# Performance work log

Measured on AMD Instinct MI355X. Metric: run time of the kernel, lower is better.

Reference implementation:

```python
import jax, jax.numpy as jnp
import numpy as np

B, S, E, H = 4, 2048, 2048, 16
D = E // H  # head_dim = 128
MAX_LEN = 2048


def _make_freqs():
    # standard RoPE frequencies: theta = 10000^{-2i/D}
    inv_freq = 1.0 / (10000.0 ** (np.arange(0, D, 2, dtype=np.float32) / D))  # [D/2]
    t = np.arange(MAX_LEN, dtype=np.float32)
    ang = np.outer(t, inv_freq)  # [max_len, D/2]
    cos = ang.reshape(1, MAX_LEN, 1, D // 2)
    return jnp.asarray(np.cos(cos)), jnp.asarray(np.sin(cos))


def setup_inputs() -> dict:
    key = jax.random.key(0)
    ks = jax.random.split(key, 10)
    sc = 1.0 / np.sqrt(E)
    freqs_cos, freqs_sin = _make_freqs()
    return {
        "x": jax.random.normal(ks[0], (B, S, E), dtype=jnp.float32),
        "freqs_cos": freqs_cos,
        "freqs_sin": freqs_sin,
        "wq": jax.random.normal(ks[1], (E, E), dtype=jnp.float32) * sc,
        "bq": jax.random.normal(ks[2], (E,), dtype=jnp.float32) * 0.01,
        "wk": jax.random.normal(ks[3], (E, E), dtype=jnp.float32) * sc,
        "bk": jax.random.normal(ks[4], (E,), dtype=jnp.float32) * 0.01,
        "wv": jax.random.normal(ks[5], (E, E), dtype=jnp.float32) * sc,
        "bv": jax.random.normal(ks[6], (E,), dtype=jnp.float32) * 0.01,
        "wo": jax.random.normal(ks[7], (E, E), dtype=jnp.float32) * sc,
        "bo": jax.random.normal(ks[8], (E,), dtype=jnp.float32) * 0.01,
    }


def _rope(t, cos, sin):
    # t: [B, S, H, D]; complex multiply on interleaved (even, odd) pairs
    tr = t.reshape(*t.shape[:-1], -1, 2)  # [B,S,H,D/2,2]
    xr, xi = tr[..., 0], tr[..., 1]
    rr = xr * cos - xi * sin
    ri = xr * sin + xi * cos
    return jnp.stack([rr, ri], axis=-1).reshape(t.shape)


def reference(x, freqs_cos, freqs_sin, wq, bq, wk, bk, wv, bv, wo, bo):
    b, s, _ = x.shape
    q = (x @ wq.T + bq).reshape(b, s, H, D)
    k = (x @ wk.T + bk).reshape(b, s, H, D)
    v = (x @ wv.T + bv).reshape(b, s, H, D)
    cos, sin = freqs_cos[:, :s], freqs_sin[:, :s]
    q = _rope(q, cos, sin)
    k = _rope(k, cos, sin)
    # FAITHFUL to source: q,k,v stay [B,S,H,D], so matmul contracts over D
    # producing per-position head-head scores [B,S,H,H] (no transpose to BHSD).
    qk = jnp.einsum("bshd,bsgd->bshg", q, k) / jnp.sqrt(jnp.float32(D))
    att = jax.nn.softmax(qk, axis=-1)
    att_out = jnp.einsum("bshg,bsgd->bshd", att, v)  # [B,S,H,D]
    # torch: transpose(1,2).contiguous().view(B,S,-1) -> h-major flatten
    att_out = jnp.transpose(att_out, (0, 2, 1, 3)).reshape(b, s, -1)
    return att_out @ wo.T + bo
```

## Files before the change

### kernel.cpp

```cpp
#include <hip/hip_runtime.h>
#include <stdint.h>

typedef unsigned short u16t;
typedef __attribute__((ext_vector_type(8))) short frag8;
typedef __attribute__((ext_vector_type(4))) float facc4;

#define S_LEN 2048
#define E_DIM 2048

__device__ __forceinline__ u16t f2bf(float f) {
    union { float f; uint32_t u; } c; c.f = f;
    return (u16t)((c.u + 0x7fffu + ((c.u >> 16) & 1u)) >> 16);
}

__global__ __launch_bounds__(256) void cvt_kernel(const float* __restrict__ src,
                                                  u16t* __restrict__ dst, int n4) {
    int i = blockIdx.x * 256 + threadIdx.x;
    if (i >= n4) return;
    float4 v = ((const float4*)src)[i];
    ushort4 o;
    o.x = f2bf(v.x); o.y = f2bf(v.y); o.z = f2bf(v.z); o.w = f2bf(v.w);
    ((ushort4*)dst)[i] = o;
}

__device__ __forceinline__ void gldl16(const u16t* g, u16t* l) {
    __builtin_amdgcn_global_load_lds(
        (__attribute__((address_space(1))) void*)(g),
        (__attribute__((address_space(3))) void*)(l), 16, 0, 0);
}

__device__ __forceinline__ void gemm256(const u16t* __restrict__ A,
                                        const u16t* __restrict__ B,
                                        int bm0, int bn0,
                                        u16t* L, facc4 acc[8][4]) {
    const int t     = threadIdx.x;
    const int lane  = t & 63;
    const int wid   = t >> 6;
    const int m16   = lane & 15;
    const int quad  = lane >> 4;
    const int wid_m = wid >> 2;
    const int wid_n = wid & 3;

#pragma unroll
    for (int i = 0; i < 8; ++i)
#pragma unroll
        for (int j = 0; j < 4; ++j) acc[i][j] = facc4{0.f, 0.f, 0.f, 0.f};

    const int colA = (((wid_m << 2) + quad) ^ (m16 & 7)) << 3;
    const int colB = ((((wid_n >> 1) << 2) + quad) ^ (m16 & 7)) << 3;
    const int roA  = m16 * 64 + colA;
    const int roB  = ((wid_n & 1) * 64 + m16) * 64 + colB;

    const int cp    = (lane & 7) ^ (lane >> 3);
    const int rgrp  = cp >> 2;
    const int qq    = cp & 3;
    const int line0 = wid * 8 + (lane >> 3);
    const u16t* pA[2]; const u16t* pB[2];
    const int dOf0 = wid * 512;
    const int dOf1 = 4096 + wid * 512;
#pragma unroll
    for (int ld = 0; ld < 2; ++ld) {
        const int grow = rgrp * 128 + ld * 64 + line0;
        pA[ld] = A + (size_t)(bm0 + grow) * E_DIM + qq * 8;
        pB[ld] = B + (size_t)(bn0 + grow) * E_DIM + qq * 8;
    }

#define STG(P, K, DST) { gldl16(P[0] + (K), (DST) + dOf0); \
                         gldl16(P[1] + (K), (DST) + dOf1); }
#define CBAR { asm volatile("" ::: "memory"); \
               __builtin_amdgcn_s_barrier(); \
               asm volatile("" ::: "memory"); }
#define RDB(BASE) { _Pragma("unroll") \
    for (int j = 0; j < 4; ++j) bv[j] = *(const frag8*)((BASE) + roB + j * 1024); }
#define RDA0(BASE) { _Pragma("unroll") \
    for (int i = 0; i < 4; ++i) av[i] = *(const frag8*)((BASE) + roA + i * 1024); }
#define RDA4(BASE) { _Pragma("unroll") \
    for (int i = 0; i < 4; ++i) av[i] = *(const frag8*)((BASE) + roA + (i + 4) * 1024); }
#define MFMA16(IB) { __builtin_amdgcn_s_setprio(1); \
    _Pragma("unroll") for (int i = 0; i < 4; ++i) \
    _Pragma("unroll") for (int j = 0; j < 4; ++j) \
        acc[i + IB][j] = __builtin_amdgcn_mfma_f32_16x16x32_bf16( \
            av[i], bv[j], acc[i + IB][j], 0, 0, 0); \
    __builtin_amdgcn_s_setprio(0); }

    STG(pB, 0,  L + 16384)
    STG(pA, 0,  L + 0)
    STG(pB, 32, L + 24576)
    STG(pA, 32, L + 8192)
    STG(pB, 64, L + 32768 + 16384)
    STG(pA, 64, L + 32768)
    STG(pB, 96, L + 32768 + 24576)
    asm volatile("s_waitcnt vmcnt(6)" ::: "memory");
    CBAR

#pragma unroll 1
    for (int u = 0; u < 16; ++u) {
        const int kO1 = u * 128 + 96;
        const int kE2 = (u < 15) ? u * 128 + 128 : 0;
        const int kO2 = (u < 15) ? u * 128 + 192 : 0;
        frag8 av[4], bv[4];

        RDB(L + 16384) RDA0(L)
        STG(pA, kO1, L + 32768 + 8192)
        CBAR MFMA16(0) CBAR

        RDA4(L)
        STG(pB, kE2, L + 16384)
        CBAR MFMA16(4) CBAR

        RDB(L + 24576) RDA0(L + 8192)
        STG(pA, kE2, L)
        CBAR MFMA16(0) CBAR

        RDA4(L + 8192)
        STG(pB, kE2 + 32, L + 24576)
        asm volatile("s_waitcnt vmcnt(6)" ::: "memory");
        CBAR MFMA16(4) CBAR

        RDB(L + 32768 + 16384) RDA0(L + 32768)
        STG(pA, kE2 + 32, L + 8192)
        CBAR MFMA16(0) CBAR

        RDA4(L + 32768)
        STG(pB, kO2, L + 32768 + 16384)
        CBAR MFMA16(4) CBAR

        RDB(L + 32768 + 24576) RDA0(L + 32768 + 8192)
        STG(pA, kO2, L + 32768)
        CBAR MFMA16(0) CBAR

        RDA4(L + 32768 + 8192)
        STG(pB, kO2 + 32, L + 32768 + 24576)
        asm volatile("s_waitcnt vmcnt(6)" ::: "memory");
        CBAR MFMA16(4) CBAR
    }

    asm volatile("s_waitcnt vmcnt(0)" ::: "memory");

#undef STG
#undef CBAR
#undef RDB
#undef RDA0
#undef RDA4
#undef MFMA16
}

__device__ __forceinline__ void tile_swz(int& bm0, int& bn0) {
    const int orig = blockIdx.y * 8 + blockIdx.x;
    const int swz  = (orig & 7) * 32 + (orig >> 3);
    bm0 = (swz >> 3) * 256;
    bn0 = (swz & 7) * 256;
}

struct QkvArgs {
    const u16t* w[3];
    const float* bias[3];
    u16t* out[3];
};

__global__ __launch_bounds__(512, 2)
void qkv_gemm(const u16t* __restrict__ xb, QkvArgs args,
              const float* __restrict__ fcos, const float* __restrict__ fsin) {
    __shared__ u16t lds[65536];
    facc4 acc[8][4];
    int bm0, bn0; tile_swz(bm0, bn0);
    const int z = blockIdx.z;
    gemm256(xb, args.w[z], bm0, bn0, lds, acc);

    const int t     = threadIdx.x;
    const int lane  = t & 63;
    const int m16   = lane & 15;
    const int quad  = lane >> 4;
    const int wid   = t >> 6;
    const int wid_m = wid >> 2;
    const int wid_n = wid & 3;
    const bool rope = (z < 2);
    u16t* out = args.out[z];
    const float* bias = args.bias[z];

#pragma unroll
    for (int i = 0; i < 8; ++i) {
#pragma unroll
        for (int j = 0; j < 4; ++j) {
            const int n = bn0 + wid_n * 64 + j * 16 + m16;
            const float bn_ = bias[n];
#pragma unroll
            for (int r = 0; r < 4; ++r) {
                const int m = bm0 + wid_m * 128 + i * 16 + quad * 4 + r;
                float v = acc[i][j][r] + bn_;
                const float part = __shfl_xor(v, 1, 64);
                if (rope) {
                    const int s = m & (S_LEN - 1);
                    const int p = (n & 127) >> 1;
                    const float cs = fcos[s * 64 + p];
                    const float sn = fsin[s * 64 + p];
                    v = (n & 1) ? (part * sn + v * cs) : (v * cs - part * sn);
                }
                out[(size_t)m * E_DIM + n] = f2bf(v);
            }
        }
    }
}

__global__ __launch_bounds__(512, 2)
void out_gemm(const u16t* __restrict__ sh, const u16t* __restrict__ wob,
              const float* __restrict__ bo, float* __restrict__ out) {
    __shared__ u16t lds[65536];
    facc4 acc[8][4];
    int bm0, bn0; tile_swz(bm0, bn0);
    gemm256(sh, wob, bm0, bn0, lds, acc);

    const int t     = threadIdx.x;
    const int lane  = t & 63;
    const int m16   = lane & 15;
    const int quad  = lane >> 4;
    const int wid   = t >> 6;
    const int wid_m = wid >> 2;
    const int wid_n = wid & 3;

#pragma unroll
    for (int i = 0; i < 8; ++i) {
#pragma unroll
        for (int j = 0; j < 4; ++j) {
            const int n = bn0 + wid_n * 64 + j * 16 + m16;
            const float bn_ = bo[n];
#pragma unroll
            for (int r = 0; r < 4; ++r) {
                const int m = bm0 + wid_m * 128 + i * 16 + quad * 4 + r;
                out[(size_t)m * E_DIM + n] = acc[i][j][r] + bn_;
            }
        }
    }
}

__global__ __launch_bounds__(256)
void attn_kernel(const u16t* __restrict__ qb, const u16t* __restrict__ kb,
                 const u16t* __restrict__ vb, u16t* __restrict__ sh) {
    __shared__ u16t Vs[4][16 * 136];
    __shared__ u16t Pt[4][16 * 32];

    const int t    = threadIdx.x;
    const int wid  = t >> 6;
    const int lane = t & 63;
    const int m16  = lane & 15;
    const int quad = lane >> 4;
    const int tk   = blockIdx.x * 4 + wid;
    const int b    = tk >> 11;
    const int s    = tk & (S_LEN - 1);
    const size_t row = (size_t)tk * E_DIM;

    frag8 aq[4], ak[4];
    const u16t* qrow = qb + row + m16 * 128 + quad * 8;
    const u16t* krow = kb + row + m16 * 128 + quad * 8;
#pragma unroll
    for (int ks = 0; ks < 4; ++ks) {
        aq[ks] = *(const frag8*)(qrow + ks * 32);
        ak[ks] = *(const frag8*)(krow + ks * 32);
    }

    u16t* vs = Vs[wid];
#pragma unroll
    for (int c = 0; c < 4; ++c) {
        const int e  = c * 512 + lane * 8;
        const int vr = e >> 7, vc = e & 127;
        *(uint4*)(vs + vr * 136 + vc) = *(const uint4*)(vb + row + e);
    }

    facc4 sacc = facc4{0.f, 0.f, 0.f, 0.f};
#pragma unroll
    for (int ks = 0; ks < 4; ++ks)
        sacc = __builtin_amdgcn_mfma_f32_16x16x32_bf16(aq[ks], ak[ks], sacc, 0, 0, 0);

    float p[4], mx[4], sm[4];
#pragma unroll
    for (int r = 0; r < 4; ++r) { p[r] = sacc[r] * 0.08838834764831845f; mx[r] = p[r]; }
#pragma unroll
    for (int msk = 1; msk < 16; msk <<= 1)
#pragma unroll
        for (int r = 0; r < 4; ++r) mx[r] = fmaxf(mx[r], __shfl_xor(mx[r], msk, 64));
#pragma unroll
    for (int r = 0; r < 4; ++r) { p[r] = __expf(p[r] - mx[r]); sm[r] = p[r]; }
#pragma unroll
    for (int msk = 1; msk < 16; msk <<= 1)
#pragma unroll
        for (int r = 0; r < 4; ++r) sm[r] += __shfl_xor(sm[r], msk, 64);

    u16t* pt = Pt[wid];
#pragma unroll
    for (int r = 0; r < 4; ++r)
        pt[(quad * 4 + r) * 32 + m16] = f2bf(p[r] / sm[r]);
    *(uint2*)(pt + m16 * 32 + 16 + quad * 4) = uint2{0u, 0u};

    __syncthreads();

    const frag8 aP = *(const frag8*)(pt + m16 * 32 + quad * 8);

    facc4 oacc[8];
#pragma unroll
    for (int d = 0; d < 8; ++d) oacc[d] = facc4{0.f, 0.f, 0.f, 0.f};
#pragma unroll
    for (int dblk = 0; dblk < 8; ++dblk) {
        union { u16t u[8]; frag8 f; } bb;
#pragma unroll
        for (int j = 0; j < 8; ++j)
            bb.u[j] = vs[((quad * 8 + j) & 15) * 136 + dblk * 16 + m16];
        oacc[dblk] = __builtin_amdgcn_mfma_f32_16x16x32_bf16(aP, bb.f, oacc[dblk], 0, 0, 0);
    }

    const size_t base = ((size_t)b << 22) + (size_t)(s >> 4) * E_DIM
                      + (size_t)((s & 15) * 128);
#pragma unroll
    for (int dblk = 0; dblk < 8; ++dblk) {
        const int d = dblk * 16 + m16;
#pragma unroll
        for (int r = 0; r < 4; ++r) {
            const int h = quad * 4 + r;
            sh[base + ((size_t)h << 18) + d] = f2bf(oacc[dblk][r]);
        }
    }
}

extern "C" void kernel_launch(void* const* d_in, const int* in_sizes, int n_in,
                              void* d_out, int out_size, void* d_ws, size_t ws_size,
                              hipStream_t stream) {
    const float* x    = (const float*)d_in[0];
    const float* fcos = (const float*)d_in[1];
    const float* fsin = (const float*)d_in[2];
    const float* wq   = (const float*)d_in[3];
    const float* bq   = (const float*)d_in[4];
    const float* wk   = (const float*)d_in[5];
    const float* bk   = (const float*)d_in[6];
    const float* wv   = (const float*)d_in[7];
    const float* bv   = (const float*)d_in[8];
    const float* wo   = (const float*)d_in[9];
    const float* bo   = (const float*)d_in[10];
    float* out = (float*)d_out;

    char* ws = (char*)d_ws;
    u16t* xb  = (u16t*)(ws);
    u16t* qb  = (u16t*)(ws + 33554432ull);
    u16t* kb  = (u16t*)(ws + 67108864ull);
    u16t* vb  = (u16t*)(ws + 100663296ull);
    u16t* wqb = (u16t*)(ws + 134217728ull);
    u16t* wkb = (u16t*)(ws + 142606336ull);
    u16t* wvb = (u16t*)(ws + 150994944ull);
    u16t* wob = (u16t*)(ws + 159383552ull);

    cvt_kernel<<<16384, 256, 0, stream>>>(x, xb, 4194304);
    cvt_kernel<<<4096, 256, 0, stream>>>(wq, wqb, 1048576);
    cvt_kernel<<<4096, 256, 0, stream>>>(wk, wkb, 1048576);
    cvt_kernel<<<4096, 256, 0, stream>>>(wv, wvb, 1048576);
    cvt_kernel<<<4096, 256, 0, stream>>>(wo, wob, 1048576);

    QkvArgs qa;
    qa.w[0] = wqb; qa.w[1] = wkb; qa.w[2] = wvb;
    qa.bias[0] = bq; qa.bias[1] = bk; qa.bias[2] = bv;
    qa.out[0] = qb; qa.out[1] = kb; qa.out[2] = vb;
    qkv_gemm<<<dim3(8, 32, 3), 512, 0, stream>>>(xb, qa, fcos, fsin);

    attn_kernel<<<2048, 256, 0, stream>>>(qb, kb, vb, xb);

    out_gemm<<<dim3(8, 32), 512, 0, stream>>>(xb, wob, bo, out);
}
```

Before: 492.6 us.

## Double-buffer LDS fragment registers to overlap reads with MFMA in GEMM mainloop

The GEMM mainloop now uses two sets of A and B fragment registers, so LDS reads for the next sub-step are issued before the MFMAs of the current one. This removes one of the two barriers around each MFMA block. The goal is to hide LDS read latency and barrier stalls behind matrix compute. In exchange it raises VGPR pressure, which could hurt occupancy under launch_bounds(512,2), and the reordered barriers and waitcnts must still keep LDS reuse race-free.

```diff
diff --git a/kernel.cpp b/kernel.cpp
--- a/kernel.cpp
+++ b/kernel.cpp
@@ -65,22 +65,23 @@
         pB[ld] = B + (size_t)(bn0 + grow) * E_DIM + qq * 8;
     }
 
+    frag8 avA[4], avB[4], bv0[4], bv1[4];
+
 #define STG(P, K, DST) { gldl16(P[0] + (K), (DST) + dOf0); \
                          gldl16(P[1] + (K), (DST) + dOf1); }
-#define CBAR { asm volatile("" ::: "memory"); \
+#define BARR { asm volatile("" ::: "memory"); \
                __builtin_amdgcn_s_barrier(); \
                asm volatile("" ::: "memory"); }
-#define RDB(BASE) { _Pragma("unroll") \
-    for (int j = 0; j < 4; ++j) bv[j] = *(const frag8*)((BASE) + roB + j * 1024); }
-#define RDA0(BASE) { _Pragma("unroll") \
-    for (int i = 0; i < 4; ++i) av[i] = *(const frag8*)((BASE) + roA + i * 1024); }
-#define RDA4(BASE) { _Pragma("unroll") \
-    for (int i = 0; i < 4; ++i) av[i] = *(const frag8*)((BASE) + roA + (i + 4) * 1024); }
-#define MFMA16(IB) { __builtin_amdgcn_s_setprio(1); \
+#define VM6 asm volatile("s_waitcnt vmcnt(6)" ::: "memory");
+#define RDB(DST, BASE) { _Pragma("unroll") \
+    for (int j = 0; j < 4; ++j) DST[j] = *(const frag8*)((BASE) + roB + j * 1024); }
+#define RDA(DST, BASE, IO) { _Pragma("unroll") \
+    for (int i = 0; i < 4; ++i) DST[i] = *(const frag8*)((BASE) + roA + ((IO) + i) * 1024); }
+#define MFMA16(IB, AV, BV) { __builtin_amdgcn_s_setprio(1); \
     _Pragma("unroll") for (int i = 0; i < 4; ++i) \
     _Pragma("unroll") for (int j = 0; j < 4; ++j) \
         acc[i + IB][j] = __builtin_amdgcn_mfma_f32_16x16x32_bf16( \
-            av[i], bv[j], acc[i + IB][j], 0, 0, 0); \
+            AV[i], BV[j], acc[i + IB][j], 0, 0, 0); \
     __builtin_amdgcn_s_setprio(0); }
 
     STG(pB, 0,  L + 16384)
@@ -90,58 +91,73 @@
     STG(pB, 64, L + 32768 + 16384)
     STG(pA, 64, L + 32768)
     STG(pB, 96, L + 32768 + 24576)
-    asm volatile("s_waitcnt vmcnt(6)" ::: "memory");
-    CBAR
+    VM6
+    BARR
+    RDB(bv0, L + 16384)
+    RDA(avA, L + 0, 0)
 
 #pragma unroll 1
     for (int u = 0; u < 16; ++u) {
         const int kO1 = u * 128 + 96;
         const int kE2 = (u < 15) ? u * 128 + 128 : 0;
         const int kO2 = (u < 15) ? u * 128 + 192 : 0;
-        frag8 av[4], bv[4];
-
-        RDB(L + 16384) RDA0(L)
+
+        BARR
+        RDA(avB, L + 0, 4)
         STG(pA, kO1, L + 32768 + 8192)
-        CBAR MFMA16(0) CBAR
-
-        RDA4(L)
+        MFMA16(0, avA, bv0)
+
+        VM6
+        BARR
+        RDB(bv1, L + 24576)
+        RDA(avA, L + 8192, 0)
         STG(pB, kE2, L + 16384)
-        CBAR MFMA16(4) CBAR
-
-        RDB(L + 24576) RDA0(L + 8192)
-        STG(pA, kE2, L)
-        CBAR MFMA16(0) CBAR
-
-        RDA4(L + 8192)
+        MFMA16(4, avB, bv0)
+
+        BARR
+        RDA(avB, L + 8192, 4)
+        STG(pA, kE2, L + 0)
+        MFMA16(0, avA, bv1)
+
+        VM6
+        BARR
+        RDB(bv0, L + 32768 + 16384)
+        RDA(avA, L + 32768, 0)
         STG(pB, kE2 + 32, L + 24576)
-        asm volatile("s_waitcnt vmcnt(6)" ::: "memory");
-        CBAR MFMA16(4) CBAR
-
-        RDB(L + 32768 + 16384) RDA0(L + 32768)
+        MFMA16(4, avB, bv1)
+
+        BARR
+        RDA(avB, L + 32768, 4)
         STG(pA, kE2 + 32, L + 8192)
-        CBAR MFMA16(0) CBAR
-
-        RDA4(L + 32768)
+        MFMA16(0, avA, bv0)
+
+        VM6
+        BARR
+        RDB(bv1, L + 32768 + 24576)
+        RDA(avA, L + 32768 + 8192, 0)
         STG(pB, kO2, L + 32768 + 16384)
-        CBAR MFMA16(4) CBAR
-
-        RDB(L + 32768 + 24576) RDA0(L + 32768 + 8192)
+        MFMA16(4, avB, bv0)
+
+        BARR
+        RDA(avB, L + 32768 + 8192, 4)
         STG(pA, kO2, L + 32768)
-        CBAR MFMA16(0) CBAR
-
-        RDA4(L + 32768 + 8192)
+        MFMA16(0, avA, bv1)
+
+        VM6
+        BARR
+        RDB(bv0, L + 16384)
+        RDA(avA, L + 0, 0)
         STG(pB, kO2 + 32, L + 32768 + 24576)
-        asm volatile("s_waitcnt vmcnt(6)" ::: "memory");
-        CBAR MFMA16(4) CBAR
+        MFMA16(4, avB, bv1)
     }
 
     asm volatile("s_waitcnt vmcnt(0)" ::: "memory");
 
 #undef STG
-#undef CBAR
+#undef BARR
+#undef VM6
 #undef RDB
-#undef RDA0
-#undef RDA4
+#undef RDA
 #undef MFMA16
 }
 
```

After: 491.5 us. No clear change (-0.2%).
